# Optimization experiments

Measured on AMD Instinct MI355X. Metric: run time of the kernel, lower is better.

## Reference

```python
import jax, jax.numpy as jnp
import numpy as np

N = 10000      # nodes (docstring: dense mode intended for <=10k nodes)
D_IN = 64      # in_dim
D_OUT = 64     # out_dim


def setup_inputs() -> dict:
    key = jax.random.key(0)
    kH, kA1, kA2, kA3, kW1, kW2, kW3 = jax.random.split(key, 7)
    H = jax.random.normal(kH, (N, D_IN), dtype=jnp.float32)
    # Dense normalized adjacency per edge type (values in [0,1), as in A_norm)
    A_r1 = jax.random.uniform(kA1, (N, N), dtype=jnp.float32)
    A_r2 = jax.random.uniform(kA2, (N, N), dtype=jnp.float32)
    A_r3 = jax.random.uniform(kA3, (N, N), dtype=jnp.float32)
    # Xavier-uniform init for type-specific linear weights [out_dim, in_dim]
    limit = float(np.sqrt(6.0 / (D_IN + D_OUT)))
    W1 = jax.random.uniform(kW1, (D_OUT, D_IN), dtype=jnp.float32, minval=-limit, maxval=limit)
    W2 = jax.random.uniform(kW2, (D_OUT, D_IN), dtype=jnp.float32, minval=-limit, maxval=limit)
    W3 = jax.random.uniform(kW3, (D_OUT, D_IN), dtype=jnp.float32, minval=-limit, maxval=limit)
    bias = jnp.zeros((D_OUT,), dtype=jnp.float32)
    return {"H": H, "A_r1": A_r1, "A_r2": A_r2, "A_r3": A_r3,
            "W1": W1, "W2": W2, "W3": W3, "bias": bias}


def reference(H, A_r1, A_r2, A_r3, W1, W2, W3, bias):
    # h_v = sum_r W_r @ (sum_u A_r[v,u] * h_u) + b  (no activation in forward)
    out = bias  # broadcasts to [N, D_OUT]
    for A_r, W_r in ((A_r1, W1), (A_r2, W2), (A_r3, W3)):
        msg = A_r @ H                      # [N, D_IN] neighbor aggregation
        out = out + msg @ W_r.T            # [N, D_OUT] type-specific projection
    return out
```

## Files before the change

kernel.cpp:

```cpp
#include <hip/hip_runtime.h>

static constexpr int NN = 10000;
static constexpr int DD = 64;
static constexpr int KP = 10240;
static constexpr int BK = 128;
static constexpr int NIT = 79;
static constexpr int BM = 64;
static constexpr int LDSROW = 136;

typedef __attribute__((ext_vector_type(4))) float f32x4;
typedef __attribute__((ext_vector_type(8))) short s16x8;

__device__ __forceinline__ unsigned short f2bf(float f) {
  unsigned u = __float_as_uint(f);
  return (unsigned short)((u + 0x7fffu + ((u >> 16) & 1u)) >> 16);
}

__global__ void prep_kernel(const float* __restrict__ H,
                            const float* __restrict__ W1,
                            const float* __restrict__ W2,
                            const float* __restrict__ W3,
                            unsigned short* __restrict__ mt) {
  const int r = blockIdx.y;
  const float* W = (r == 0) ? W1 : (r == 1) ? W2 : W3;
  const int wave = threadIdx.x >> 6;
  const int lane = threadIdx.x & 63;
  f32x4 wr[16];
#pragma unroll
  for (int i = 0; i < 16; ++i) wr[i] = *(const f32x4*)&W[lane * 64 + i * 4];
  unsigned short* orow = mt + ((size_t)r * 64 + lane) * KP;
  const int kbase = blockIdx.x * 128 + wave * 32;
  for (int i = 0; i < 32; ++i) {
    const int k = kbase + i;
    if (k < NN) {
      float s = 0.f;
#pragma unroll
      for (int j = 0; j < 16; ++j) {
        f32x4 h = *(const f32x4*)&H[(size_t)k * 64 + j * 4];
        s += h[0] * wr[j][0] + h[1] * wr[j][1] + h[2] * wr[j][2] + h[3] * wr[j][3];
      }
      orow[k] = f2bf(s);
    } else {
      orow[k] = 0;
    }
  }
}

__global__ void init_out_kernel(const float* __restrict__ bias, float* __restrict__ out) {
  const int i = blockIdx.x * 256 + threadIdx.x;
  if (i < NN * DD) out[i] = bias[i & 63];
}

__global__ __launch_bounds__(256) void gcn_main(const float* __restrict__ A1,
                                                const float* __restrict__ A2,
                                                const float* __restrict__ A3,
                                                const unsigned short* __restrict__ mt,
                                                float* __restrict__ out) {
  __shared__ __align__(16) unsigned short mlds[2 * 64 * LDSROW];

  const int r = blockIdx.y;
  const float* A = (r == 0) ? A1 : (r == 1) ? A2 : A3;
  const unsigned short* mtr = mt + (size_t)r * 64 * KP;

  const int wave = threadIdx.x >> 6;
  const int lane = threadIdx.x & 63;
  const int l15 = lane & 15;
  const int lhi = lane >> 4;
  const int v0 = blockIdx.x * BM;

  int vA = v0 + wave * 16 + l15;
  if (vA > NN - 1) vA = NN - 1;
  const float* arow = A + (size_t)vA * NN;

  const int srow = wave * 16 + l15;
  const int sseg = lhi;
  const unsigned short* mrow = mtr + (size_t)srow * KP + sseg * 32;

  f32x4 acc[4] = {{0.f,0.f,0.f,0.f},{0.f,0.f,0.f,0.f},{0.f,0.f,0.f,0.f},{0.f,0.f,0.f,0.f}};
  f32x4 aF[4][2], aN[4][2];
  s16x8 mS[4];

  auto loadM = [&](int t) {
#pragma unroll
    for (int j = 0; j < 4; ++j) mS[j] = *(const s16x8*)(mrow + (size_t)t * BK + j * 8);
  };
  auto writeM = [&](int buf) {
    unsigned short* base = &mlds[buf * 64 * LDSROW + srow * LDSROW];
#pragma unroll
    for (int j = 0; j < 4; ++j) *(s16x8*)(base + (sseg * 4 + j) * 8) = mS[j];
  };
  auto loadA = [&](f32x4 (&a)[4][2], int t, bool guard) {
    const int kb = t * BK;
#pragma unroll
    for (int kk = 0; kk < 4; ++kk) {
      const int kf = kb + kk * 32 + lhi * 8;
      if (!guard) {
        a[kk][0] = *(const f32x4*)(arow + kf);
        a[kk][1] = *(const f32x4*)(arow + kf + 4);
      } else {
        f32x4 z = {0.f, 0.f, 0.f, 0.f};
        a[kk][0] = (kf < NN) ? *(const f32x4*)(arow + kf) : z;
        a[kk][1] = (kf + 4 < NN) ? *(const f32x4*)(arow + kf + 4) : z;
      }
    }
  };
  auto cvtA = [&](const f32x4& x, const f32x4& y) -> s16x8 {
    s16x8 v;
    v[0] = (short)f2bf(x[0]); v[1] = (short)f2bf(x[1]);
    v[2] = (short)f2bf(x[2]); v[3] = (short)f2bf(x[3]);
    v[4] = (short)f2bf(y[0]); v[5] = (short)f2bf(y[1]);
    v[6] = (short)f2bf(y[2]); v[7] = (short)f2bf(y[3]);
    return v;
  };

  loadM(0);
  loadA(aF, 0, false);
  writeM(0);
  __syncthreads();

  for (int t = 0; t < NIT; ++t) {
    const int buf = t & 1;
    const bool pref = (t + 1 < NIT);
    if (pref) {
      loadM(t + 1);
      loadA(aN, t + 1, (t + 1 == NIT - 1));
    }
#pragma unroll
    for (int kk = 0; kk < 4; ++kk) {
      s16x8 a = cvtA(aF[kk][0], aF[kk][1]);
#pragma unroll
      for (int dt = 0; dt < 4; ++dt) {
        s16x8 b = *(const s16x8*)&mlds[buf * 64 * LDSROW + (dt * 16 + l15) * LDSROW + (kk * 4 + lhi) * 8];
        acc[dt] = __builtin_amdgcn_mfma_f32_16x16x32_bf16(a, b, acc[dt], 0, 0, 0);
      }
    }
    if (pref) writeM(buf ^ 1);
    __syncthreads();
    if (pref) {
#pragma unroll
      for (int kk = 0; kk < 4; ++kk) { aF[kk][0] = aN[kk][0]; aF[kk][1] = aN[kk][1]; }
    }
  }

#pragma unroll
  for (int dt = 0; dt < 4; ++dt) {
    const int d = dt * 16 + l15;
#pragma unroll
    for (int i = 0; i < 4; ++i) {
      const int v = v0 + wave * 16 + lhi * 4 + i;
      if (v < NN) atomicAdd(&out[(size_t)v * DD + d], acc[dt][i]);
    }
  }
}

extern "C" void kernel_launch(void* const* d_in, const int* in_sizes, int n_in,
                              void* d_out, int out_size, void* d_ws, size_t ws_size,
                              hipStream_t stream) {
  const float* H    = (const float*)d_in[0];
  const float* A1   = (const float*)d_in[1];
  const float* A2   = (const float*)d_in[2];
  const float* A3   = (const float*)d_in[3];
  const float* W1   = (const float*)d_in[4];
  const float* W2   = (const float*)d_in[5];
  const float* W3   = (const float*)d_in[6];
  const float* bias = (const float*)d_in[7];
  float* out = (float*)d_out;
  unsigned short* mt = (unsigned short*)d_ws;

  prep_kernel<<<dim3(KP / 128, 3), 256, 0, stream>>>(H, W1, W2, W3, mt);
  init_out_kernel<<<dim3((NN * DD + 255) / 256), 256, 0, stream>>>(bias, out);
  gcn_main<<<dim3((NN + BM - 1) / BM, 3), 256, 0, stream>>>(A1, A2, A3, mt, out);
}
```

Measured before the change: 328.7 us.

## Split K across blocks and read projected features directly from global memory

Adds an 8-way split of the reduction dimension across a new grid axis, so the grid grows from 471 to about 3768 blocks and the atomic adds combine the partial sums. It also drops the LDS double buffer and block barriers for the bf16 projected-feature matrix. Each wave now loads its B fragments straight from global/L2 every iteration. This is meant to fill more of the GPU's compute units and remove synchronisation stalls, at the cost of redundant global loads of the small matrix and eight times as many atomics on the output.

```diff
diff --git a/kernel.cpp b/kernel.cpp
--- a/kernel.cpp
+++ b/kernel.cpp
@@ -4,9 +4,10 @@
 static constexpr int DD = 64;
 static constexpr int KP = 10240;
 static constexpr int BK = 128;
-static constexpr int NIT = 79;
+static constexpr int SPLITS = 8;
+static constexpr int KC = KP / SPLITS;
+static constexpr int ITERS = KC / BK;
 static constexpr int BM = 64;
-static constexpr int LDSROW = 136;
 
 typedef __attribute__((ext_vector_type(4))) float f32x4;
 typedef __attribute__((ext_vector_type(8))) short s16x8;
@@ -56,9 +57,8 @@
                                                 const float* __restrict__ A3,
                                                 const unsigned short* __restrict__ mt,
                                                 float* __restrict__ out) {
-  __shared__ __align__(16) unsigned short mlds[2 * 64 * LDSROW];
-
-  const int r = blockIdx.y;
+  const int r = blockIdx.z;
+  const int s = blockIdx.y;
   const float* A = (r == 0) ? A1 : (r == 1) ? A2 : A3;
   const unsigned short* mtr = mt + (size_t)r * 64 * KP;
 
@@ -67,30 +67,17 @@
   const int l15 = lane & 15;
   const int lhi = lane >> 4;
   const int v0 = blockIdx.x * BM;
+  const int k0 = s * KC;
 
   int vA = v0 + wave * 16 + l15;
   if (vA > NN - 1) vA = NN - 1;
   const float* arow = A + (size_t)vA * NN;
 
-  const int srow = wave * 16 + l15;
-  const int sseg = lhi;
-  const unsigned short* mrow = mtr + (size_t)srow * KP + sseg * 32;
-
   f32x4 acc[4] = {{0.f,0.f,0.f,0.f},{0.f,0.f,0.f,0.f},{0.f,0.f,0.f,0.f},{0.f,0.f,0.f,0.f}};
   f32x4 aF[4][2], aN[4][2];
-  s16x8 mS[4];
 
-  auto loadM = [&](int t) {
-#pragma unroll
-    for (int j = 0; j < 4; ++j) mS[j] = *(const s16x8*)(mrow + (size_t)t * BK + j * 8);
-  };
-  auto writeM = [&](int buf) {
-    unsigned short* base = &mlds[buf * 64 * LDSROW + srow * LDSROW];
-#pragma unroll
-    for (int j = 0; j < 4; ++j) *(s16x8*)(base + (sseg * 4 + j) * 8) = mS[j];
-  };
-  auto loadA = [&](f32x4 (&a)[4][2], int t, bool guard) {
-    const int kb = t * BK;
+  auto loadA = [&](f32x4 (&a)[4][2], int kb) {
+    const bool guard = (kb + BK > NN);
 #pragma unroll
     for (int kk = 0; kk < 4; ++kk) {
       const int kf = kb + kk * 32 + lhi * 8;
@@ -99,8 +86,12 @@
         a[kk][1] = *(const f32x4*)(arow + kf + 4);
       } else {
         f32x4 z = {0.f, 0.f, 0.f, 0.f};
-        a[kk][0] = (kf < NN) ? *(const f32x4*)(arow + kf) : z;
-        a[kk][1] = (kf + 4 < NN) ? *(const f32x4*)(arow + kf + 4) : z;
+        if (kf < NN) {
+          a[kk][0] = *(const f32x4*)(arow + kf);
+          a[kk][1] = *(const f32x4*)(arow + kf + 4);
+        } else {
+          a[kk][0] = z; a[kk][1] = z;
+        }
       }
     }
   };
@@ -113,29 +104,28 @@
     return v;
   };
 
-  loadM(0);
-  loadA(aF, 0, false);
-  writeM(0);
-  __syncthreads();
+  loadA(aF, k0);
 
-  for (int t = 0; t < NIT; ++t) {
-    const int buf = t & 1;
-    const bool pref = (t + 1 < NIT);
-    if (pref) {
-      loadM(t + 1);
-      loadA(aN, t + 1, (t + 1 == NIT - 1));
-    }
+#pragma unroll 2
+  for (int t = 0; t < ITERS; ++t) {
+    const int kb = k0 + t * BK;
+    const bool pref = (t + 1 < ITERS);
+    if (pref) loadA(aN, kb + BK);
+
+    s16x8 b[4][4];
+#pragma unroll
+    for (int kk = 0; kk < 4; ++kk)
+#pragma unroll
+      for (int dt = 0; dt < 4; ++dt)
+        b[kk][dt] = *(const s16x8*)(mtr + (size_t)(dt * 16 + l15) * KP + kb + (kk * 4 + lhi) * 8);
+
 #pragma unroll
     for (int kk = 0; kk < 4; ++kk) {
       s16x8 a = cvtA(aF[kk][0], aF[kk][1]);
 #pragma unroll
-      for (int dt = 0; dt < 4; ++dt) {
-        s16x8 b = *(const s16x8*)&mlds[buf * 64 * LDSROW + (dt * 16 + l15) * LDSROW + (kk * 4 + lhi) * 8];
-        acc[dt] = __builtin_amdgcn_mfma_f32_16x16x32_bf16(a, b, acc[dt], 0, 0, 0);
-      }
+      for (int dt = 0; dt < 4; ++dt)
+        acc[dt] = __builtin_amdgcn_mfma_f32_16x16x32_bf16(a, b[kk][dt], acc[dt], 0, 0, 0);
     }
-    if (pref) writeM(buf ^ 1);
-    __syncthreads();
     if (pref) {
 #pragma unroll
       for (int kk = 0; kk < 4; ++kk) { aF[kk][0] = aN[kk][0]; aF[kk][1] = aN[kk][1]; }
@@ -169,5 +159,5 @@
 
   prep_kernel<<<dim3(KP / 128, 3), 256, 0, stream>>>(H, W1, W2, W3, mt);
   init_out_kernel<<<dim3((NN * DD + 255) / 256), 256, 0, stream>>>(bias, out);
-  gcn_main<<<dim3((NN + BM - 1) / BM, 3), 256, 0, stream>>>(A1, A2, A3, mt, out);
+  gcn_main<<<dim3((NN + BM - 1) / BM, SPLITS, 3), 256, 0, stream>>>(A1, A2, A3, mt, out);
 }
```

Measured after the change: 479.8 us. +46.0%, slower.
